# Kernel tuning notes

Measured on AMD Instinct MI355X. Metric: run time of the kernel, lower is better.

## Reference

```python
import jax, jax.numpy as jnp
import numpy as np

MD = 4                  # corr_md
D = 2 * MD + 1          # patch_size = 9


def setup_inputs() -> dict:
    key = jax.random.key(0)
    k1, k2 = jax.random.split(key)
    b, c, h, w = 4, 128, 128, 256
    t1 = jax.random.normal(k1, (b, c, h, w), dtype=jnp.float32)
    t2 = jax.random.normal(k2, (b, c, h, w), dtype=jnp.float32)
    return {"t1": t1, "t2": t2}


def reference(t1, t2):
    # Local cost volume: for each displacement (di, dj) in [-MD, MD]^2,
    # out[b, p, y, x] = sum_c t1[b, c, y, x] * t2[b, c, y+di, x+dj]
    # with zero padding outside t2 (SpatialCorrelationSampler semantics,
    # kernel_size=1, stride=1, dilation_patch=1; no channel normalization).
    b, c, h, w = t1.shape
    t2p = jnp.pad(t2, ((0, 0), (0, 0), (MD, MD), (MD, MD)))
    # Loop over the fixed 9x9 displacement grid (81 small reductions);
    outs = [
        jnp.einsum('bchw,bchw->bhw', t1, t2p[:, :, i:i + h, j:j + w])
        for i in range(D) for j in range(D)
    ]
    return jnp.stack(outs, axis=1)  # [b, 81, h, w]
```

## Files before the change

### kernel.cpp

```cpp
#include <hip/hip_runtime.h>

#define NP 81
#define CC 128
#define HH 128
#define WW 256
#define YP 136
#define XP 288
#define WS_NEED 40108032ull

typedef __attribute__((ext_vector_type(8))) short short8;
typedef __attribute__((ext_vector_type(4))) float f32x4;
typedef __attribute__((ext_vector_type(16))) float f32x16;

__device__ __forceinline__ short f2bf(float f) {
    unsigned int u = __builtin_bit_cast(unsigned int, f);
    u += 0x7fffu + ((u >> 16) & 1u);
    return (short)(u >> 16);
}

__global__ __launch_bounds__(256) void prepass_t2(const float* __restrict__ t2,
                                                  short* __restrict__ ws) {
    const int u = blockIdx.x * 256 + threadIdx.x;
    const int xp = u % XP;
    const int v  = u / XP;
    const int yp = v % YP;
    const int bc = v / YP;
    const int y2 = yp - 4, x2 = xp - 4;
    short8 lo = {0,0,0,0,0,0,0,0}, hi = {0,0,0,0,0,0,0,0};
    if (y2 >= 0 && y2 < HH && x2 >= 0 && x2 < WW) {
        const int b = bc >> 3, cg = bc & 7;
        const size_t pl = (size_t)HH * WW;
        const float* p = t2 + ((size_t)(b * CC + cg * 16) * HH + y2) * WW + x2;
#pragma unroll
        for (int j = 0; j < 8; j++) lo[j] = f2bf(p[(size_t)j * pl]);
#pragma unroll
        for (int j = 0; j < 8; j++) hi[j] = f2bf(p[(size_t)(j + 8) * pl]);
    }
    short* o = ws + (size_t)u * 16;
    *(short8*)o = lo;
    *(short8*)(o + 8) = hi;
}

__global__ __launch_bounds__(576, 7) void corr32_v2(const float* __restrict__ t1,
                                                    const short* __restrict__ ws,
                                                    float* __restrict__ out) {
    const int id = blockIdx.x;
    const int xt = id & 7;
    const int y  = (id >> 3) & (HH - 1);
    const int b  = id >> 10;
    const int X0 = xt * 32;

    const int tid  = threadIdx.x;
    const int lane = tid & 63;
    const int w    = tid >> 6;
    const int n    = lane & 31;
    const int g    = lane >> 5;

    __shared__ float smemf[3240];
    short* sA = (short*)smemf;

    const size_t plane = (size_t)HH * WW;

    if (tid < 512) {
        const int x = tid & 31, oct = tid >> 5;
        const float* p = t1 + (size_t)(b * CC + oct * 8) * plane
                       + (size_t)y * WW + X0 + x;
        short8 pk;
#pragma unroll
        for (int j = 0; j < 8; j++) pk[j] = f2bf(p[(size_t)j * plane]);
        *(short8*)&sA[x * 128 + ((oct ^ (x & 15)) * 8)] = pk;
    }

    f32x16 acc[2];
#pragma unroll
    for (int t = 0; t < 2; ++t)
#pragma unroll
        for (int r = 0; r < 16; ++r) acc[t][r] = 0.f;

    const size_t cstride = (size_t)YP * XP * 16;
    size_t bofs = ((((size_t)b * 8) * YP + (y + w)) * XP + (X0 + n)) * 16 + g * 8;

    short8 c0 = *(const short8*)(ws + bofs);
    short8 c1 = *(const short8*)(ws + bofs + 512);

    __syncthreads();

#pragma unroll
    for (int kc = 0; kc < 8; ++kc) {
        short8 p0, p1;
        if (kc < 7) {
            p0 = *(const short8*)(ws + bofs + cstride);
            p1 = *(const short8*)(ws + bofs + cstride + 512);
        }
        const short8 af = *(const short8*)
            &sA[n * 128 + (((kc * 2 + g) ^ (n & 15)) * 8)];
        acc[0] = __builtin_amdgcn_mfma_f32_32x32x16_bf16(af, c0, acc[0], 0, 0, 0);
        acc[1] = __builtin_amdgcn_mfma_f32_32x32x16_bf16(af, c1, acc[1], 0, 0, 0);
        if (kc < 7) { c0 = p0; c1 = p1; bofs += cstride; }
    }

    __syncthreads();
    float* obuf = smemf;
#pragma unroll
    for (int t = 0; t < 2; ++t)
#pragma unroll
        for (int r = 0; r < 16; ++r) {
            const int m  = (r & 3) + 8 * (r >> 2) + 4 * g;
            const int dj = n - m + 32 * t;
            if (dj >= 0 && dj <= 8) obuf[(w * 9 + dj) * 40 + m] = acc[t][r];
        }
    __syncthreads();
    for (int u = tid; u < 648; u += 576) {
        const int p = u >> 3, xq = u & 7;
        f32x4 v = *(const f32x4*)&obuf[p * 40 + xq * 4];
        *(f32x4*)&out[((size_t)(b * NP + p) * HH + y) * WW + X0 + xq * 4] = v;
    }
}

__global__ __launch_bounds__(256) void corr_mfma_kernel(
        const float* __restrict__ t1, const float* __restrict__ t2,
        float* __restrict__ out) {
    const int id = blockIdx.x;
    const int xt = id & 3;
    const int y  = (id >> 2) & (HH - 1);
    const int b  = id >> 9;
    const int X0 = xt * 64;
    const int tid  = threadIdx.x;
    const int lane = tid & 63;
    const int wv   = tid >> 6;
    const int n    = lane & 15;
    const int q    = lane >> 4;
    __shared__ short smem[2560 + 28800];
    short* sA = smem;
    short* sB = smem + 2560;
    f32x4 acc[9][2];
#pragma unroll
    for (int i = 0; i < 9; i++)
#pragma unroll
        for (int t = 0; t < 2; t++) acc[i][t] = (f32x4){0.f, 0.f, 0.f, 0.f};
    const size_t plane = (size_t)HH * WW;
    const float* t1b = t1 + (size_t)b * CC * plane + (size_t)y * WW;
    const float* t2b = t2 + (size_t)b * CC * plane;
    for (int c0 = 0; c0 < CC; c0 += 32) {
        __syncthreads();
        {
            const int x  = tid & 63;
            const int cg = tid >> 6;
            const float* p = t1b + (size_t)(c0 + cg * 8) * plane + X0 + x;
            short8 pk;
#pragma unroll
            for (int j = 0; j < 8; j++) pk[j] = f2bf(p[(size_t)j * plane]);
            *(short8*)&sA[x * 40 + cg * 8] = pk;
        }
#pragma unroll
        for (int i = 0; i < 12; i++) {
            const int u = tid + i * 256;
            if (u < 2880) {
                const int r   = u / 320;
                const int rem = u - r * 320;
                const int cg  = rem / 80;
                const int ix  = rem - cg * 80;
                const int y2  = y + r - 4;
                const int x2  = X0 - 4 + ix;
                short8 pk;
                if (y2 >= 0 && y2 < HH && x2 >= 0 && x2 < WW) {
                    const float* p = t2b + (size_t)(c0 + cg * 8) * plane
                                   + (size_t)y2 * WW + x2;
#pragma unroll
                    for (int j = 0; j < 8; j++) pk[j] = f2bf(p[(size_t)j * plane]);
                } else {
#pragma unroll
                    for (int j = 0; j < 8; j++) pk[j] = 0;
                }
                *(short8*)&sB[r * 3200 + ix * 40 + cg * 8] = pk;
            }
        }
        __syncthreads();
        const short8 af = *(const short8*)&sA[(16 * wv + n) * 40 + q * 8];
#pragma unroll
        for (int di = 0; di < 9; di++) {
#pragma unroll
            for (int t = 0; t < 2; t++) {
                const short8 bf = *(const short8*)
                    &sB[di * 3200 + (16 * wv + 16 * t + n) * 40 + q * 8];
                acc[di][t] = __builtin_amdgcn_mfma_f32_16x16x32_bf16(
                    af, bf, acc[di][t], 0, 0, 0);
            }
        }
    }
    __syncthreads();
    float* obuf = (float*)smem;
#pragma unroll
    for (int di = 0; di < 9; di++)
#pragma unroll
        for (int t = 0; t < 2; t++)
#pragma unroll
            for (int r = 0; r < 4; r++) {
                const int m  = q * 4 + r;
                const int dj = n - m + 16 * t;
                if (dj >= 0 && dj <= 8)
                    obuf[(di * 9 + dj) * 68 + 16 * wv + m] = acc[di][t][r];
            }
    __syncthreads();
    float* ob = out + (size_t)b * NP * plane + (size_t)y * WW + X0;
#pragma unroll
    for (int i = 0; i < 6; i++) {
        const int u = tid + i * 256;
        if (u < 1296) {
            const int p  = u >> 4;
            const int xu = u & 15;
            f32x4 v = *(const f32x4*)&obuf[p * 68 + xu * 4];
            *(f32x4*)&ob[(size_t)p * plane + xu * 4] = v;
        }
    }
}

extern "C" void kernel_launch(void* const* d_in, const int* in_sizes, int n_in,
                              void* d_out, int out_size, void* d_ws, size_t ws_size,
                              hipStream_t stream) {
    const float* t1 = (const float*)d_in[0];
    const float* t2 = (const float*)d_in[1];
    float* out = (float*)d_out;
    if (ws_size >= WS_NEED) {
        short* ws = (short*)d_ws;
        prepass_t2<<<4896, 256, 0, stream>>>(t2, ws);
        corr32_v2<<<4096, 576, 0, stream>>>(t1, ws, out);
    } else {
        corr_mfma_kernel<<<2048, 256, 0, stream>>>(t1, t2, out);
    }
}
```

Measured before the change: 194.6 us.

## Fuse t2 prepass into single kernel with 8-row strips and register-resident t2 rows

```diff
diff --git a/kernel.cpp b/kernel.cpp
--- a/kernel.cpp
+++ b/kernel.cpp
@@ -4,9 +4,6 @@
 #define CC 128
 #define HH 128
 #define WW 256
-#define YP 136
-#define XP 288
-#define WS_NEED 40108032ull
 
 typedef __attribute__((ext_vector_type(8))) short short8;
 typedef __attribute__((ext_vector_type(4))) float f32x4;
@@ -18,37 +15,16 @@
     return (short)(u >> 16);
 }
 
-__global__ __launch_bounds__(256) void prepass_t2(const float* __restrict__ t2,
-                                                  short* __restrict__ ws) {
-    const int u = blockIdx.x * 256 + threadIdx.x;
-    const int xp = u % XP;
-    const int v  = u / XP;
-    const int yp = v % YP;
-    const int bc = v / YP;
-    const int y2 = yp - 4, x2 = xp - 4;
-    short8 lo = {0,0,0,0,0,0,0,0}, hi = {0,0,0,0,0,0,0,0};
-    if (y2 >= 0 && y2 < HH && x2 >= 0 && x2 < WW) {
-        const int b = bc >> 3, cg = bc & 7;
-        const size_t pl = (size_t)HH * WW;
-        const float* p = t2 + ((size_t)(b * CC + cg * 16) * HH + y2) * WW + x2;
-#pragma unroll
-        for (int j = 0; j < 8; j++) lo[j] = f2bf(p[(size_t)j * pl]);
-#pragma unroll
-        for (int j = 0; j < 8; j++) hi[j] = f2bf(p[(size_t)(j + 8) * pl]);
-    }
-    short* o = ws + (size_t)u * 16;
-    *(short8*)o = lo;
-    *(short8*)(o + 8) = hi;
-}
-
-__global__ __launch_bounds__(576, 7) void corr32_v2(const float* __restrict__ t1,
-                                                    const short* __restrict__ ws,
-                                                    float* __restrict__ out) {
-    const int id = blockIdx.x;
-    const int xt = id & 7;
-    const int y  = (id >> 3) & (HH - 1);
-    const int b  = id >> 10;
+__global__ __launch_bounds__(1024) void corr_fused(
+        const float* __restrict__ t1, const float* __restrict__ t2,
+        float* __restrict__ out) {
+    const int bid = blockIdx.x;
+    const int sw  = (bid & 7) * 64 + (bid >> 3);
+    const int xt    = sw & 7;
+    const int strip = (sw >> 3) & 15;
+    const int b     = sw >> 7;
     const int X0 = xt * 32;
+    const int y0 = strip * 8;
 
     const int tid  = threadIdx.x;
     const int lane = tid & 63;
@@ -56,161 +32,101 @@
     const int n    = lane & 31;
     const int g    = lane >> 5;
 
-    __shared__ float smemf[3240];
-    short* sA = (short*)smemf;
+    __shared__ short sA[8 * 32 * 128];
+    __shared__ float obufs[16 * 9 * 36];
 
     const size_t plane = (size_t)HH * WW;
+    const int r = y0 - 4 + w;
 
-    if (tid < 512) {
-        const int x = tid & 31, oct = tid >> 5;
-        const float* p = t1 + (size_t)(b * CC + oct * 8) * plane
-                       + (size_t)y * WW + X0 + x;
-        short8 pk;
+    short8 bre[8][2];
+    {
+        const bool rok = (r >= 0) && (r < HH);
 #pragma unroll
-        for (int j = 0; j < 8; j++) pk[j] = f2bf(p[(size_t)j * plane]);
-        *(short8*)&sA[x * 128 + ((oct ^ (x & 15)) * 8)] = pk;
-    }
-
-    f32x16 acc[2];
+        for (int t = 0; t < 2; ++t) {
+            const int x2 = X0 - 4 + n + 32 * t;
+            if (rok && x2 >= 0 && x2 < WW) {
+                const float* p = t2 + ((size_t)(b * CC + g * 8) * HH + r) * WW + x2;
 #pragma unroll
-    for (int t = 0; t < 2; ++t)
+                for (int kc = 0; kc < 8; ++kc) {
+                    short8 f;
 #pragma unroll
-        for (int r = 0; r < 16; ++r) acc[t][r] = 0.f;
-
-    const size_t cstride = (size_t)YP * XP * 16;
-    size_t bofs = ((((size_t)b * 8) * YP + (y + w)) * XP + (X0 + n)) * 16 + g * 8;
-
-    short8 c0 = *(const short8*)(ws + bofs);
-    short8 c1 = *(const short8*)(ws + bofs + 512);
-
-    __syncthreads();
-
+                    for (int j = 0; j < 8; ++j)
+                        f[j] = f2bf(p[(size_t)(kc * 16 + j) * plane]);
+                    bre[kc][t] = f;
+                }
+            } else {
 #pragma unroll
-    for (int kc = 0; kc < 8; ++kc) {
-        short8 p0, p1;
-        if (kc < 7) {
-            p0 = *(const short8*)(ws + bofs + cstride);
-            p1 = *(const short8*)(ws + bofs + cstride + 512);
-        }
-        const short8 af = *(const short8*)
-            &sA[n * 128 + (((kc * 2 + g) ^ (n & 15)) * 8)];
-        acc[0] = __builtin_amdgcn_mfma_f32_32x32x16_bf16(af, c0, acc[0], 0, 0, 0);
-        acc[1] = __builtin_amdgcn_mfma_f32_32x32x16_bf16(af, c1, acc[1], 0, 0, 0);
-        if (kc < 7) { c0 = p0; c1 = p1; bofs += cstride; }
-    }
-
-    __syncthreads();
-    float* obuf = smemf;
-#pragma unroll
-    for (int t = 0; t < 2; ++t)
-#pragma unroll
-        for (int r = 0; r < 16; ++r) {
-            const int m  = (r & 3) + 8 * (r >> 2) + 4 * g;
-            const int dj = n - m + 32 * t;
-            if (dj >= 0 && dj <= 8) obuf[(w * 9 + dj) * 40 + m] = acc[t][r];
-        }
-    __syncthreads();
-    for (int u = tid; u < 648; u += 576) {
-        const int p = u >> 3, xq = u & 7;
-        f32x4 v = *(const f32x4*)&obuf[p * 40 + xq * 4];
-        *(f32x4*)&out[((size_t)(b * NP + p) * HH + y) * WW + X0 + xq * 4] = v;
-    }
-}
-
-__global__ __launch_bounds__(256) void corr_mfma_kernel(
-        const float* __restrict__ t1, const float* __restrict__ t2,
-        float* __restrict__ out) {
-    const int id = blockIdx.x;
-    const int xt = id & 3;
-    const int y  = (id >> 2) & (HH - 1);
-    const int b  = id >> 9;
-    const int X0 = xt * 64;
-    const int tid  = threadIdx.x;
-    const int lane = tid & 63;
-    const int wv   = tid >> 6;
-    const int n    = lane & 15;
-    const int q    = lane >> 4;
-    __shared__ short smem[2560 + 28800];
-    short* sA = smem;
-    short* sB = smem + 2560;
-    f32x4 acc[9][2];
-#pragma unroll
-    for (int i = 0; i < 9; i++)
-#pragma unroll
-        for (int t = 0; t < 2; t++) acc[i][t] = (f32x4){0.f, 0.f, 0.f, 0.f};
-    const size_t plane = (size_t)HH * WW;
-    const float* t1b = t1 + (size_t)b * CC * plane + (size_t)y * WW;
-    const float* t2b = t2 + (size_t)b * CC * plane;
-    for (int c0 = 0; c0 < CC; c0 += 32) {
-        __syncthreads();
-        {
-            const int x  = tid & 63;
-            const int cg = tid >> 6;
-            const float* p = t1b + (size_t)(c0 + cg * 8) * plane + X0 + x;
-            short8 pk;
-#pragma unroll
-            for (int j = 0; j < 8; j++) pk[j] = f2bf(p[(size_t)j * plane]);
-            *(short8*)&sA[x * 40 + cg * 8] = pk;
-        }
-#pragma unroll
-        for (int i = 0; i < 12; i++) {
-            const int u = tid + i * 256;
-            if (u < 2880) {
-                const int r   = u / 320;
-                const int rem = u - r * 320;
-                const int cg  = rem / 80;
-                const int ix  = rem - cg * 80;
-                const int y2  = y + r - 4;
-                const int x2  = X0 - 4 + ix;
-                short8 pk;
-                if (y2 >= 0 && y2 < HH && x2 >= 0 && x2 < WW) {
-                    const float* p = t2b + (size_t)(c0 + cg * 8) * plane
-                                   + (size_t)y2 * WW + x2;
-#pragma unroll
-                    for (int j = 0; j < 8; j++) pk[j] = f2bf(p[(size_t)j * plane]);
-                } else {
-#pragma unroll
-                    for (int j = 0; j < 8; j++) pk[j] = 0;
-                }
-                *(short8*)&sB[r * 3200 + ix * 40 + cg * 8] = pk;
-            }
-        }
-        __syncthreads();
-        const short8 af = *(const short8*)&sA[(16 * wv + n) * 40 + q * 8];
-#pragma unroll
-        for (int di = 0; di < 9; di++) {
-#pragma unroll
-            for (int t = 0; t < 2; t++) {
-                const short8 bf = *(const short8*)
-                    &sB[di * 3200 + (16 * wv + 16 * t + n) * 40 + q * 8];
-                acc[di][t] = __builtin_amdgcn_mfma_f32_16x16x32_bf16(
-                    af, bf, acc[di][t], 0, 0, 0);
+                for (int kc = 0; kc < 8; ++kc)
+                    bre[kc][t] = (short8){0,0,0,0,0,0,0,0};
             }
         }
     }
+
+#pragma unroll
+    for (int i = 0; i < 4; ++i) {
+        const int unit = tid + i * 1024;
+        const int x   = unit & 31;
+        const int oct = (unit >> 5) & 15;
+        const int yy  = unit >> 9;
+        const float* p = t1 + ((size_t)(b * CC + oct * 8) * HH + (y0 + yy)) * WW
+                       + X0 + x;
+        short8 pk;
+#pragma unroll
+        for (int j = 0; j < 8; ++j) pk[j] = f2bf(p[(size_t)j * plane]);
+        *(short8*)&sA[yy * 4096 + x * 128 + ((oct ^ (x & 15)) * 8)] = pk;
+    }
     __syncthreads();
-    float* obuf = (float*)smem;
+
+    const int ylo = (w > 8) ? (w - 8) : 0;
+    const int yhi = (w < 7) ? w : 7;
+    float* ob = &obufs[w * 324];
+
+    for (int yy = ylo; yy <= yhi; ++yy) {
+        const int sbase = yy * 4096 + n * 128;
+
+        f32x16 a0;
 #pragma unroll
-    for (int di = 0; di < 9; di++)
+        for (int q = 0; q < 16; ++q) a0[q] = 0.f;
 #pragma unroll
-        for (int t = 0; t < 2; t++)
+        for (int kc = 0; kc < 8; ++kc) {
+            const short8 af = *(const short8*)
+                &sA[sbase + (((kc * 2 + g) ^ (n & 15)) * 8)];
+            a0 = __builtin_amdgcn_mfma_f32_32x32x16_bf16(af, bre[kc][0], a0, 0, 0, 0);
+        }
 #pragma unroll
-            for (int r = 0; r < 4; r++) {
-                const int m  = q * 4 + r;
-                const int dj = n - m + 16 * t;
-                if (dj >= 0 && dj <= 8)
-                    obuf[(di * 9 + dj) * 68 + 16 * wv + m] = acc[di][t][r];
+        for (int q = 0; q < 16; ++q) {
+            const int m  = (q & 3) + 8 * (q >> 2) + 4 * g;
+            const int dj = n - m;
+            if (dj >= 0 && dj <= 8) ob[dj * 36 + m] = a0[q];
+        }
+
+        f32x16 a1;
+#pragma unroll
+        for (int q = 0; q < 16; ++q) a1[q] = 0.f;
+#pragma unroll
+        for (int kc = 0; kc < 8; ++kc) {
+            const short8 af = *(const short8*)
+                &sA[sbase + (((kc * 2 + g) ^ (n & 15)) * 8)];
+            a1 = __builtin_amdgcn_mfma_f32_32x32x16_bf16(af, bre[kc][1], a1, 0, 0, 0);
+        }
+#pragma unroll
+        for (int q = 0; q < 16; ++q) {
+            const int m  = (q & 3) + 8 * (q >> 2) + 4 * g;
+            const int dj = n - m + 32;
+            if (dj >= 0 && dj <= 8) ob[dj * 36 + m] = a1[q];
+        }
+
+        const int di = w - yy;
+        const int y  = y0 + yy;
+        float* obase = out + ((size_t)(b * NP + di * 9) * HH + y) * WW + X0;
+#pragma unroll
+        for (int k = 0; k < 2; ++k) {
+            const int u = lane + k * 64;
+            if (u < 72) {
+                const int dj = u >> 3, xq = u & 7;
+                f32x4 v = *(const f32x4*)&ob[dj * 36 + xq * 4];
+                *(f32x4*)&obase[(size_t)dj * plane + xq * 4] = v;
             }
-    __syncthreads();
-    float* ob = out + (size_t)b * NP * plane + (size_t)y * WW + X0;
-#pragma unroll
-    for (int i = 0; i < 6; i++) {
-        const int u = tid + i * 256;
-        if (u < 1296) {
-            const int p  = u >> 4;
-            const int xu = u & 15;
-            f32x4 v = *(const f32x4*)&obuf[p * 68 + xu * 4];
-            *(f32x4*)&ob[(size_t)p * plane + xu * 4] = v;
         }
     }
 }
@@ -220,12 +136,5 @@
                               hipStream_t stream) {
     const float* t1 = (const float*)d_in[0];
     const float* t2 = (const float*)d_in[1];
-    float* out = (float*)d_out;
-    if (ws_size >= WS_NEED) {
-        short* ws = (short*)d_ws;
-        prepass_t2<<<4896, 256, 0, stream>>>(t2, ws);
-        corr32_v2<<<4096, 576, 0, stream>>>(t1, ws, out);
-    } else {
-        corr_mfma_kernel<<<2048, 256, 0, stream>>>(t1, t2, out);
-    }
+    corr_fused<<<512, 1024, 0, stream>>>(t1, t2, (float*)d_out);
 }
```

Result: slower. 225.4 us (+15.8%).
